# Kernel tuning notes

Hardware: AMD Instinct MI355X
Metric: run time of the kernel (lower is better)

## Reference

```python
import jax, jax.numpy as jnp
import numpy as np

DEP_NUM, HEAD_NUM, BSZ, DIM, REL = 96, 96, 16, 512, 128


def setup_inputs() -> dict:
    key = jax.random.key(0)
    k1, k2, k3, k4 = jax.random.split(key, 4)
    outs = jax.random.normal(k1, (DEP_NUM, BSZ, DIM), dtype=jnp.float32)
    graph_state = jax.random.normal(k2, (HEAD_NUM, BSZ, DIM), dtype=jnp.float32)
    # nn.init.normal_(std=0.02) for both weights, zero biases
    Wt = 0.02 * jax.random.normal(k3, (DIM, 2 * DIM), dtype=jnp.float32)
    bt = jnp.zeros((DIM,), dtype=jnp.float32)
    Wp = 0.02 * jax.random.normal(k4, (REL, DIM), dtype=jnp.float32)
    bp = jnp.zeros((REL,), dtype=jnp.float32)
    return {"outs": outs, "graph_state": graph_state, "Wt": Wt, "bt": bt, "Wp": Wp, "bp": bp}


def reference(outs, graph_state, Wt, bt, Wp, bp):
    # outs: [dep, b, D], graph_state: [head, b, D]
    # Linear(cat(dep, head)) == dep @ Wt[:, :D].T + head @ Wt[:, D:].T + bt
    D = outs.shape[-1]
    dep_proj = jnp.einsum('dbi,ei->dbe', outs, Wt[:, :D])           # [dep, b, D]
    head_proj = jnp.einsum('hbi,ei->hbe', graph_state, Wt[:, D:])   # [head, b, D]
    # broadcast-sum to pairwise: [dep, b, head, D]
    h = jax.nn.relu(dep_proj[:, :, None, :] + jnp.swapaxes(head_proj, 0, 1)[None] + bt)
    # dropout: identity in eval mode
    scores = jnp.einsum('dbhe,re->dbhr', h, Wp) + bp                # [dep, b, head, REL]
    nil = jnp.zeros(scores.shape[:-1] + (1,), dtype=scores.dtype)
    scores = jnp.concatenate([nil, scores], axis=-1)                # [dep, b, head, REL+1]
    return jax.nn.log_softmax(scores, axis=-1)
```

## Files before the change

kernel.cpp:

```cpp
#include <hip/hip_runtime.h>
#include <math.h>

#define DEP   96
#define HEADS 96
#define BSZ   16
#define DIM   512
#define REL   128
#define RELP  129

typedef __attribute__((ext_vector_type(8))) _Float16  half8;
typedef __attribute__((ext_vector_type(2))) __fp16    fp16x2;
typedef __attribute__((ext_vector_type(4))) float     floatx4;

__device__ __forceinline__ unsigned short f2h(float x) {
    union { _Float16 h; unsigned short u; } c;
    c.h = (_Float16)x;
    return c.u;
}
__device__ __forceinline__ unsigned pk_f2h(float a, float b) {
    union { fp16x2 h; unsigned u; } c;
    c.h = __builtin_amdgcn_cvt_pkrtz(a, b);
    return c.u;
}
__device__ __forceinline__ unsigned pk_add_h2(unsigned a, unsigned b) {
    unsigned r; asm("v_pk_add_f16 %0, %1, %2" : "=v"(r) : "v"(a), "v"(b)); return r;
}
__device__ __forceinline__ unsigned pk_max_h2(unsigned a, unsigned b) {
    unsigned r; asm("v_pk_max_f16 %0, %1, %2" : "=v"(r) : "v"(a), "v"(b)); return r;
}

#define PSS 72

__global__ __launch_bounds__(256) void proj_kernel(
    const float* __restrict__ outs, const float* __restrict__ graph,
    const float* __restrict__ Wt, const float* __restrict__ bt,
    const float* __restrict__ Wp,
    float* __restrict__ P1, unsigned short* __restrict__ P2H,
    unsigned short* __restrict__ WpH)
{
    {
        const int fb = (blockIdx.z * gridDim.y + blockIdx.y) * gridDim.x + blockIdx.x;
        if (fb < 32) {
            const int c = fb * 256 + (int)threadIdx.x;
            float4 a = *(const float4*)(Wp + (size_t)c * 8);
            float4 b = *(const float4*)(Wp + (size_t)c * 8 + 4);
            uint4 o;
            o.x = pk_f2h(a.x, a.y); o.y = pk_f2h(a.z, a.w);
            o.z = pk_f2h(b.x, b.y); o.w = pk_f2h(b.z, b.w);
            *(uint4*)(WpH + (size_t)c * 8) = o;
        }
    }

    const int z = blockIdx.z;
    const float* A = z ? graph : outs;
    const int off  = z ? DIM : 0;
    const int row0 = blockIdx.y * 32;
    const int col0 = blockIdx.x * 64;

    __shared__ __align__(16) unsigned short As[32 * PSS];
    __shared__ __align__(16) unsigned short Ws[64 * PSS];

    const int tid  = threadIdx.x;
    const int lane = tid & 63;
    const int wv   = tid >> 6;
    const int ln15 = lane & 15;
    const int quad = lane >> 4;
    const int mh   = wv & 1;
    const int nh   = wv >> 1;

    floatx4 acc[2];
    acc[0] = (floatx4){0.f,0.f,0.f,0.f};
    acc[1] = (floatx4){0.f,0.f,0.f,0.f};

    for (int kt = 0; kt < DIM; kt += 64) {
        {
            const int r  = tid >> 3;
            const int e8 = (tid & 7) * 8;
            const float* p = A + (size_t)(row0 + r) * DIM + kt + e8;
            float4 va = *(const float4*)p;
            float4 vb = *(const float4*)(p + 4);
            uint4 o;
            o.x = pk_f2h(va.x, va.y); o.y = pk_f2h(va.z, va.w);
            o.z = pk_f2h(vb.x, vb.y); o.w = pk_f2h(vb.z, vb.w);
            *(uint4*)&As[r * PSS + e8] = o;
        }
        #pragma unroll
        for (int q = 0; q < 2; ++q) {
            const int slot = q*256 + tid;
            const int r  = slot >> 3;
            const int e8 = (slot & 7) * 8;
            const float* p = Wt + (size_t)(col0 + r) * (2*DIM) + off + kt + e8;
            float4 va = *(const float4*)p;
            float4 vb = *(const float4*)(p + 4);
            uint4 o;
            o.x = pk_f2h(va.x, va.y); o.y = pk_f2h(va.z, va.w);
            o.z = pk_f2h(vb.x, vb.y); o.w = pk_f2h(vb.z, vb.w);
            *(uint4*)&Ws[r * PSS + e8] = o;
        }
        __syncthreads();
        #pragma unroll
        for (int ks = 0; ks < 64; ks += 32) {
            half8 af = *(const half8*)&As[(mh*16 + ln15) * PSS + ks + quad*8];
            #pragma unroll
            for (int nt = 0; nt < 2; ++nt) {
                half8 bf8 = *(const half8*)&Ws[(nh*32 + nt*16 + ln15) * PSS + ks + quad*8];
                acc[nt] = __builtin_amdgcn_mfma_f32_16x16x32_f16(af, bf8, acc[nt], 0, 0, 0);
            }
        }
        __syncthreads();
    }

    #pragma unroll
    for (int nt = 0; nt < 2; ++nt) {
        #pragma unroll
        for (int reg = 0; reg < 4; ++reg) {
            const int m = row0 + mh*16 + quad*4 + reg;
            const int n = col0 + nh*32 + nt*16 + ln15;
            float v = acc[nt][reg];
            if (!z) P1[(size_t)m * DIM + n] = v + bt[n];
            else    P2H[(size_t)m * DIM + n] = f2h(v);
        }
    }
}

#define HS2 40

__global__ __launch_bounds__(256, 4) void fused_kernel(
    const float* __restrict__ P1, const unsigned short* __restrict__ P2H,
    const unsigned short* __restrict__ WpH, const float* __restrict__ bp,
    float* __restrict__ out)
{
    const int db = blockIdx.x;
    const int b  = db & 15;

    __shared__ __align__(16) char arena[18944];
    unsigned short* hs    = (unsigned short*)arena;
    unsigned short* ws    = (unsigned short*)(arena + 7680);
    unsigned short* drowH = (unsigned short*)(arena + 17920);
    float* pmx  = (float*)arena;
    float* pl   = pmx + 192;
    float* lseS = pl + 192;

    const int tid  = threadIdx.x;
    const int lane = tid & 63;
    const int wv   = tid >> 6;
    const int ln15 = lane & 15;
    const int quad = lane >> 4;
    const int mh   = wv & 1;
    const int nh   = wv >> 1;
    const int e8   = (tid & 3) * 8;
    const int r0   = tid >> 2;

    {
        float2 v = *(const float2*)(P1 + (size_t)db * DIM + tid*2);
        *(unsigned*)&drowH[tid*2] = pk_f2h(v.x, v.y);
    }
    __syncthreads();

    floatx4 acc[3][4];
    #pragma unroll
    for (int i = 0; i < 3; ++i)
        #pragma unroll
        for (int j = 0; j < 4; ++j) acc[i][j] = (floatx4){0.f,0.f,0.f,0.f};

    for (int kt = 0; kt < DIM; kt += 32) {
        uint4 dv = *(const uint4*)&drowH[kt + e8];
        {
            const int h = r0;
            uint4 pv = *(const uint4*)(P2H + ((size_t)h * BSZ + b) * DIM + kt + e8);
            uint4 o;
            o.x = pk_max_h2(pk_add_h2(pv.x, dv.x), 0u);
            o.y = pk_max_h2(pk_add_h2(pv.y, dv.y), 0u);
            o.z = pk_max_h2(pk_add_h2(pv.z, dv.z), 0u);
            o.w = pk_max_h2(pk_add_h2(pv.w, dv.w), 0u);
            *(uint4*)&hs[h * HS2 + e8] = o;
        }
        if (tid < 128) {
            const int h = 64 + r0;
            uint4 pv = *(const uint4*)(P2H + ((size_t)h * BSZ + b) * DIM + kt + e8);
            uint4 o;
            o.x = pk_max_h2(pk_add_h2(pv.x, dv.x), 0u);
            o.y = pk_max_h2(pk_add_h2(pv.y, dv.y), 0u);
            o.z = pk_max_h2(pk_add_h2(pv.z, dv.z), 0u);
            o.w = pk_max_h2(pk_add_h2(pv.w, dv.w), 0u);
            *(uint4*)&hs[h * HS2 + e8] = o;
        }
        #pragma unroll
        for (int q = 0; q < 2; ++q) {
            const int r = q*64 + r0;
            *(uint4*)&ws[r * HS2 + e8] =
                *(const uint4*)(WpH + (size_t)r * DIM + kt + e8);
        }
        __syncthreads();

        {
            half8 af[3], bf[4];
            #pragma unroll
            for (int mt = 0; mt < 3; ++mt)
                af[mt] = *(const half8*)&hs[(mh*48 + mt*16 + ln15) * HS2 + quad*8];
            #pragma unroll
            for (int nt = 0; nt < 4; ++nt)
                bf[nt] = *(const half8*)&ws[(nh*64 + nt*16 + ln15) * HS2 + quad*8];
            #pragma unroll
            for (int nt = 0; nt < 4; ++nt)
                #pragma unroll
                for (int mt = 0; mt < 3; ++mt)
                    acc[mt][nt] = __builtin_amdgcn_mfma_f32_16x16x32_f16(
                        af[mt], bf[nt], acc[mt][nt], 0, 0, 0);
        }
        __syncthreads();
    }

    float bpv[4];
    #pragma unroll
    for (int nt = 0; nt < 4; ++nt) bpv[nt] = bp[nh*64 + nt*16 + ln15];

    #pragma unroll
    for (int mt = 0; mt < 3; ++mt) {
        #pragma unroll
        for (int reg = 0; reg < 4; ++reg) {
            const int m = mh*48 + mt*16 + quad*4 + reg;
            float s[4];
            #pragma unroll
            for (int nt = 0; nt < 4; ++nt) s[nt] = acc[mt][nt][reg] + bpv[nt];
            float mx = fmaxf(fmaxf(s[0], s[1]), fmaxf(s[2], s[3]));
            #pragma unroll
            for (int msk = 1; msk < 16; msk <<= 1) mx = fmaxf(mx, __shfl_xor(mx, msk));
            float l = 0.f;
            #pragma unroll
            for (int nt = 0; nt < 4; ++nt) l += __expf(s[nt] - mx);
            #pragma unroll
            for (int msk = 1; msk < 16; msk <<= 1) l += __shfl_xor(l, msk);
            if (ln15 == 0) { pmx[m*2 + nh] = mx; pl[m*2 + nh] = l; }
        }
    }
    __syncthreads();

    if (tid < 96) {
        const float mx0 = pmx[tid*2], mx1 = pmx[tid*2 + 1];
        const float MX = fmaxf(fmaxf(mx0, mx1), 0.f);
        const float L  = pl[tid*2] * __expf(mx0 - MX) + pl[tid*2 + 1] * __expf(mx1 - MX)
                       + __expf(-MX);
        lseS[tid] = MX + __logf(L);
    }
    __syncthreads();

    #pragma unroll
    for (int mt = 0; mt < 3; ++mt) {
        #pragma unroll
        for (int reg = 0; reg < 4; ++reg) {
            const int m = mh*48 + mt*16 + quad*4 + reg;
            const float lse = lseS[m];
            const size_t base = ((size_t)db * HEADS + m) * RELP;
            #pragma unroll
            for (int nt = 0; nt < 4; ++nt)
                out[base + 1 + nh*64 + nt*16 + ln15] = acc[mt][nt][reg] + bpv[nt] - lse;
            if (nh == 0 && ln15 == 0) out[base] = -lse;
        }
    }
}

extern "C" void kernel_launch(void* const* d_in, const int* in_sizes, int n_in,
                              void* d_out, int out_size, void* d_ws, size_t ws_size,
                              hipStream_t stream) {
    const float* outs  = (const float*)d_in[0];
    const float* graph = (const float*)d_in[1];
    const float* Wt    = (const float*)d_in[2];
    const float* bt    = (const float*)d_in[3];
    const float* Wp    = (const float*)d_in[4];
    const float* bp    = (const float*)d_in[5];
    float* out = (float*)d_out;

    float* P1           = (float*)d_ws;
    unsigned short* P2H = (unsigned short*)(P1 + 786432);
    unsigned short* WpH = P2H + 786432;

    proj_kernel<<<dim3(DIM/64, (DEP*BSZ)/32, 2), 256, 0, stream>>>(
        outs, graph, Wt, bt, Wp, P1, P2H, WpH);
    fused_kernel<<<DEP*BSZ, 256, 0, stream>>>(P1, P2H, WpH, bp, out);
}
```

Measured before the change: 151.3 us.

## Split fused kernel over head chunks of 32 with K-tile 64

Each block now handles 32 heads for one (dep,batch) row instead of all 96, so the grid grows to three times as many blocks. The K step widens from 32 to 64, with padded LDS strides, to halve the number of barriers. This raises parallelism and shrinks accumulator registers per thread. The cost is that the full Wp tile is reloaded three times as often per (dep,batch) row, and each wave does less MFMA work per barrier.

After: 151.9 us. About the same (+0.4%).

```diff
diff --git a/kernel.cpp b/kernel.cpp
--- a/kernel.cpp
+++ b/kernel.cpp
@@ -123,23 +123,25 @@
     }
 }
 
-#define HS2 40
+#define HSS 72
+#define WSS 72
 
 __global__ __launch_bounds__(256, 4) void fused_kernel(
     const float* __restrict__ P1, const unsigned short* __restrict__ P2H,
     const unsigned short* __restrict__ WpH, const float* __restrict__ bp,
     float* __restrict__ out)
 {
-    const int db = blockIdx.x;
+    const int m0 = blockIdx.x * 32;
+    const int db = blockIdx.y;
     const int b  = db & 15;
 
-    __shared__ __align__(16) char arena[18944];
+    __shared__ __align__(16) char arena[24064];
     unsigned short* hs    = (unsigned short*)arena;
-    unsigned short* ws    = (unsigned short*)(arena + 7680);
-    unsigned short* drowH = (unsigned short*)(arena + 17920);
+    unsigned short* ws    = (unsigned short*)(arena + 4608);
+    unsigned short* drowH = (unsigned short*)(arena + 23040);
     float* pmx  = (float*)arena;
-    float* pl   = pmx + 192;
-    float* lseS = pl + 192;
+    float* pl   = pmx + 64;
+    float* lseS = pl + 64;
 
     const int tid  = threadIdx.x;
     const int lane = tid & 63;
@@ -148,8 +150,7 @@
     const int quad = lane >> 4;
     const int mh   = wv & 1;
     const int nh   = wv >> 1;
-    const int e8   = (tid & 3) * 8;
-    const int r0   = tid >> 2;
+    const int e8   = (tid & 7) * 8;
 
     {
         float2 v = *(const float2*)(P1 + (size_t)db * DIM + tid*2);
@@ -157,56 +158,40 @@
     }
     __syncthreads();
 
-    floatx4 acc[3][4];
-    #pragma unroll
-    for (int i = 0; i < 3; ++i)
-        #pragma unroll
-        for (int j = 0; j < 4; ++j) acc[i][j] = (floatx4){0.f,0.f,0.f,0.f};
-
-    for (int kt = 0; kt < DIM; kt += 32) {
+    floatx4 acc[4];
+    #pragma unroll
+    for (int j = 0; j < 4; ++j) acc[j] = (floatx4){0.f,0.f,0.f,0.f};
+
+    for (int kt = 0; kt < DIM; kt += 64) {
         uint4 dv = *(const uint4*)&drowH[kt + e8];
         {
-            const int h = r0;
-            uint4 pv = *(const uint4*)(P2H + ((size_t)h * BSZ + b) * DIM + kt + e8);
+            const int hl = tid >> 3;
+            uint4 pv = *(const uint4*)(P2H + ((size_t)(m0 + hl) * BSZ + b) * DIM + kt + e8);
             uint4 o;
             o.x = pk_max_h2(pk_add_h2(pv.x, dv.x), 0u);
             o.y = pk_max_h2(pk_add_h2(pv.y, dv.y), 0u);
             o.z = pk_max_h2(pk_add_h2(pv.z, dv.z), 0u);
             o.w = pk_max_h2(pk_add_h2(pv.w, dv.w), 0u);
-            *(uint4*)&hs[h * HS2 + e8] = o;
-        }
-        if (tid < 128) {
-            const int h = 64 + r0;
-            uint4 pv = *(const uint4*)(P2H + ((size_t)h * BSZ + b) * DIM + kt + e8);
-            uint4 o;
-            o.x = pk_max_h2(pk_add_h2(pv.x, dv.x), 0u);
-            o.y = pk_max_h2(pk_add_h2(pv.y, dv.y), 0u);
-            o.z = pk_max_h2(pk_add_h2(pv.z, dv.z), 0u);
-            o.w = pk_max_h2(pk_add_h2(pv.w, dv.w), 0u);
-            *(uint4*)&hs[h * HS2 + e8] = o;
-        }
-        #pragma unroll
-        for (int q = 0; q < 2; ++q) {
-            const int r = q*64 + r0;
-            *(uint4*)&ws[r * HS2 + e8] =
+            *(uint4*)&hs[hl * HSS + e8] = o;
+        }
+        #pragma unroll
+        for (int q = 0; q < 4; ++q) {
+            const int r = (q*256 + tid) >> 3;
+            *(uint4*)&ws[r * WSS + e8] =
                 *(const uint4*)(WpH + (size_t)r * DIM + kt + e8);
         }
         __syncthreads();
 
-        {
-            half8 af[3], bf[4];
-            #pragma unroll
-            for (int mt = 0; mt < 3; ++mt)
-                af[mt] = *(const half8*)&hs[(mh*48 + mt*16 + ln15) * HS2 + quad*8];
+        #pragma unroll
+        for (int ks = 0; ks < 64; ks += 32) {
+            half8 af = *(const half8*)&hs[(mh*16 + ln15) * HSS + ks + quad*8];
+            half8 bf[4];
             #pragma unroll
             for (int nt = 0; nt < 4; ++nt)
-                bf[nt] = *(const half8*)&ws[(nh*64 + nt*16 + ln15) * HS2 + quad*8];
+                bf[nt] = *(const half8*)&ws[(nh*64 + nt*16 + ln15) * WSS + ks + quad*8];
             #pragma unroll
             for (int nt = 0; nt < 4; ++nt)
-                #pragma unroll
-                for (int mt = 0; mt < 3; ++mt)
-                    acc[mt][nt] = __builtin_amdgcn_mfma_f32_16x16x32_f16(
-                        af[mt], bf[nt], acc[mt][nt], 0, 0, 0);
+                acc[nt] = __builtin_amdgcn_mfma_f32_16x16x32_f16(af, bf[nt], acc[nt], 0, 0, 0);
         }
         __syncthreads();
     }
@@ -216,27 +201,24 @@
     for (int nt = 0; nt < 4; ++nt) bpv[nt] = bp[nh*64 + nt*16 + ln15];
 
     #pragma unroll
-    for (int mt = 0; mt < 3; ++mt) {
-        #pragma unroll
-        for (int reg = 0; reg < 4; ++reg) {
-            const int m = mh*48 + mt*16 + quad*4 + reg;
-            float s[4];
-            #pragma unroll
-            for (int nt = 0; nt < 4; ++nt) s[nt] = acc[mt][nt][reg] + bpv[nt];
-            float mx = fmaxf(fmaxf(s[0], s[1]), fmaxf(s[2], s[3]));
-            #pragma unroll
-            for (int msk = 1; msk < 16; msk <<= 1) mx = fmaxf(mx, __shfl_xor(mx, msk));
-            float l = 0.f;
-            #pragma unroll
-            for (int nt = 0; nt < 4; ++nt) l += __expf(s[nt] - mx);
-            #pragma unroll
-            for (int msk = 1; msk < 16; msk <<= 1) l += __shfl_xor(l, msk);
-            if (ln15 == 0) { pmx[m*2 + nh] = mx; pl[m*2 + nh] = l; }
-        }
+    for (int reg = 0; reg < 4; ++reg) {
+        const int m = mh*16 + quad*4 + reg;
+        float s[4];
+        #pragma unroll
+        for (int nt = 0; nt < 4; ++nt) s[nt] = acc[nt][reg] + bpv[nt];
+        float mx = fmaxf(fmaxf(s[0], s[1]), fmaxf(s[2], s[3]));
+        #pragma unroll
+        for (int msk = 1; msk < 16; msk <<= 1) mx = fmaxf(mx, __shfl_xor(mx, msk));
+        float l = 0.f;
+        #pragma unroll
+        for (int nt = 0; nt < 4; ++nt) l += __expf(s[nt] - mx);
+        #pragma unroll
+        for (int msk = 1; msk < 16; msk <<= 1) l += __shfl_xor(l, msk);
+        if (ln15 == 0) { pmx[m*2 + nh] = mx; pl[m*2 + nh] = l; }
     }
     __syncthreads();
 
-    if (tid < 96) {
+    if (tid < 32) {
         const float mx0 = pmx[tid*2], mx1 = pmx[tid*2 + 1];
         const float MX = fmaxf(fmaxf(mx0, mx1), 0.f);
         const float L  = pl[tid*2] * __expf(mx0 - MX) + pl[tid*2 + 1] * __expf(mx1 - MX)
@@ -246,17 +228,14 @@
     __syncthreads();
 
     #pragma unroll
-    for (int mt = 0; mt < 3; ++mt) {
-        #pragma unroll
-        for (int reg = 0; reg < 4; ++reg) {
-            const int m = mh*48 + mt*16 + quad*4 + reg;
-            const float lse = lseS[m];
-            const size_t base = ((size_t)db * HEADS + m) * RELP;
-            #pragma unroll
-            for (int nt = 0; nt < 4; ++nt)
-                out[base + 1 + nh*64 + nt*16 + ln15] = acc[mt][nt][reg] + bpv[nt] - lse;
-            if (nh == 0 && ln15 == 0) out[base] = -lse;
-        }
+    for (int reg = 0; reg < 4; ++reg) {
+        const int m = mh*16 + quad*4 + reg;
+        const float lse = lseS[m];
+        const size_t base = ((size_t)db * HEADS + m0 + m) * RELP;
+        #pragma unroll
+        for (int nt = 0; nt < 4; ++nt)
+            out[base + 1 + nh*64 + nt*16 + ln15] = acc[nt][reg] + bpv[nt] - lse;
+        if (nh == 0 && ln15 == 0) out[base] = -lse;
     }
 }
 
@@ -277,5 +256,5 @@
 
     proj_kernel<<<dim3(DIM/64, (DEP*BSZ)/32, 2), 256, 0, stream>>>(
         outs, graph, Wt, bt, Wp, P1, P2H, WpH);
-    fused_kernel<<<DEP*BSZ, 256, 0, stream>>>(P1, P2H, WpH, bp, out);
-}
+    fused_kernel<<<dim3(3, DEP*BSZ), 256, 0, stream>>>(P1, P2H, WpH, bp, out);
+}
```
